# Kernel tuning notes

Hardware: AMD Instinct MI355X
Metric: run time of the kernel (lower is better)

## Reference

```python
import jax, jax.numpy as jnp
import numpy as np

B, S, H = 2, 2048, 2304
NH, NKV, HD = 8, 4, 256
SOFTCAP = 50.0
INIT = 0.02


def setup_inputs() -> dict:
    key = jax.random.key(0)
    k1, k2, k3, k4, k5 = jax.random.split(key, 5)
    hidden_states = jax.random.normal(k1, (B, S, H), dtype=jnp.float32)
    attention_mask = jnp.ones((B, S), dtype=jnp.int32)
    position_ids = jnp.broadcast_to(jnp.arange(S, dtype=jnp.int32), (B, S))
    Wq = jax.random.normal(k2, (H, NH * HD), dtype=jnp.float32) * INIT
    Wk = jax.random.normal(k3, (H, NKV * HD), dtype=jnp.float32) * INIT
    Wv = jax.random.normal(k4, (H, NKV * HD), dtype=jnp.float32) * INIT
    Wo = jax.random.normal(k5, (NH * HD, H), dtype=jnp.float32) * INIT
    return {"hidden_states": hidden_states, "attention_mask": attention_mask,
            "position_ids": position_ids, "Wq": Wq, "Wk": Wk, "Wv": Wv, "Wo": Wo}


def _rotate_half(t):
    return jnp.concatenate([-t[..., HD // 2:], t[..., :HD // 2]], axis=-1)


def reference(hidden_states, attention_mask, position_ids, Wq, Wk, Wv, Wo):
    b, s, _ = hidden_states.shape
    # projections + head split
    q = (hidden_states @ Wq).reshape(b, s, NH, HD)
    k = (hidden_states @ Wk).reshape(b, s, NKV, HD)
    v = (hidden_states @ Wv).reshape(b, s, NKV, HD)
    # RoPE (Gemma sinusoidal table, gathered by position_ids)
    inv_freq = 1.0 / (10000.0 ** (jnp.arange(0, HD, 2, dtype=jnp.float32) / HD))
    freqs = position_ids.astype(jnp.float32)[..., None] * inv_freq      # [B,S,HD/2]
    emb = jnp.concatenate([freqs, freqs], axis=-1)                      # [B,S,HD]
    sin = jnp.sin(emb)[:, :, None, :]
    cos = jnp.cos(emb)[:, :, None, :]
    q = q * cos + _rotate_half(q) * sin
    k = k * cos + _rotate_half(k) * sin
    # GQA: repeat KV heads to match query heads
    groups = NH // NKV
    k = jnp.repeat(k, groups, axis=2)
    v = jnp.repeat(v, groups, axis=2)
    # scaled logits, mask, tanh softcap (order matches source: mask -> softcap -> softmax)
    q = q / jnp.sqrt(jnp.float32(HD))
    scores = jnp.einsum('bqhd,bkhd->bhqk', q, k)                        # [B,NH,S,S]
    causal = jnp.tril(jnp.ones((s, s), dtype=bool))
    mask = causal[None, None] & (attention_mask[:, None, None, :] > 0)
    big_neg = jnp.finfo(scores.dtype).min
    scores = jnp.where(mask, scores, big_neg)
    scores = jnp.tanh(scores / SOFTCAP) * SOFTCAP
    w = jax.nn.softmax(scores, axis=-1)
    out = jnp.einsum('bhqk,bkhd->bqhd', w, v).reshape(b, s, NH * HD)
    return out @ Wo
```

## Files before the change

### kernel.cpp

```cpp
#include <hip/hip_runtime.h>
#include <hip/hip_bf16.h>
#include <stdint.h>

typedef unsigned short u16;
typedef __attribute__((ext_vector_type(8))) short s16x8;
typedef __attribute__((ext_vector_type(4))) float f32x4;

#define B_ 2
#define S_ 2048
#define H_ 2304
#define NH_ 8
#define NKV_ 4
#define HD_ 256

__device__ __forceinline__ float bf2f(u16 u) {
  union { uint32_t i; float f; } x; x.i = ((uint32_t)u) << 16; return x.f;
}
__device__ __forceinline__ u16 f2bf(float f) {
  union { float f; uint32_t i; } x; x.f = f;
  uint32_t u = x.i;
  return (u16)((u + 0x7fffu + ((u >> 16) & 1u)) >> 16);
}
__device__ __forceinline__ u16 f2bft(float f) {
  union { float f; uint32_t i; } x; x.f = f;
  return (u16)(x.i >> 16);
}

__device__ __forceinline__ void async16(const void* g, void* l) {
  __builtin_amdgcn_global_load_lds((const __attribute__((address_space(1))) uint32_t*)g,
                                   (__attribute__((address_space(3))) uint32_t*)l, 16, 0, 0);
}

__device__ __forceinline__ f32x4 mfma16(s16x8 a, s16x8 b, f32x4 c) {
  return __builtin_amdgcn_mfma_f32_16x16x32_bf16(a, b, c, 0, 0, 0);
}

__global__ __launch_bounds__(256) void prep_kernel(
    const float* __restrict__ X, u16* __restrict__ Xb,
    const float* __restrict__ Wq, u16* __restrict__ WqT,
    const float* __restrict__ Wk, u16* __restrict__ WkT,
    const float* __restrict__ Wv, u16* __restrict__ WvT,
    const float* __restrict__ Wo, u16* __restrict__ WoT,
    float* __restrict__ ct, float* __restrict__ st) {
  __shared__ u16 tile[32][33];
  int bid = blockIdx.x, tid = threadIdx.x;

  auto tposeT = [&](const float* in, u16* out, int R, int C, int bx, int by) {
    int c0 = bx * 32, r0 = by * 32;
    int x = tid & 31, y = tid >> 5;
#pragma unroll
    for (int j = 0; j < 32; j += 8)
      tile[y + j][x] = f2bf(in[(size_t)(r0 + y + j) * C + c0 + x]);
    __syncthreads();
#pragma unroll
    for (int j = 0; j < 32; j += 8)
      out[(size_t)(c0 + y + j) * R + r0 + x] = tile[x][y + j];
  };

  if (bid < 1024) {
    int t = bid * 256 + tid;
    int d = t & 127;
    int p = t >> 7;
    float invf = exp2f(-(float)d * 0.1038102530f);
    float f = (float)p * invf;
    float s, c;
    sincosf(f, &s, &c);
    ct[t] = c;
    st[t] = s;
  } else if (bid < 10240) {
    size_t i = ((size_t)(bid - 1024) * 256 + tid) * 4;
    float4 v = *(const float4*)(X + i);
    ushort4 o;
    o.x = f2bf(v.x); o.y = f2bf(v.y); o.z = f2bf(v.z); o.w = f2bf(v.w);
    *(ushort4*)(Xb + i) = o;
  } else if (bid < 14848) {
    int b2 = bid - 10240;
    tposeT(Wq, WqT, 2304, 2048, b2 & 63, b2 >> 6);
  } else if (bid < 17152) {
    int b2 = bid - 14848;
    tposeT(Wk, WkT, 2304, 1024, b2 & 31, b2 >> 5);
  } else if (bid < 19456) {
    int b2 = bid - 17152;
    tposeT(Wv, WvT, 2304, 1024, b2 & 31, b2 >> 5);
  } else {
    int b2 = bid - 19456;
    tposeT(Wo, WoT, 2048, 2304, b2 % 72, b2 / 72);
  }
}

__global__ __launch_bounds__(256) void mid_kernel(u16* __restrict__ QKV, u16* __restrict__ VTb,
                                                  const int* __restrict__ pos_ids,
                                                  const float* __restrict__ ct,
                                                  const float* __restrict__ st) {
  __shared__ u16 tile[32][33];
  int bid = blockIdx.x, tid = threadIdx.x;
  if (bid < 1024) {
    int t = bid * 256 + tid;
    int dg = t & 15, h = (t >> 4) & 3, row = t >> 6;
    u16* p1 = QKV + (size_t)row * 4096 + 2048 + h * 256 + dg * 8;
    u16* p2 = p1 + 128;
    int pos = pos_ids[row];
    const float* ctp = ct + pos * 128 + dg * 8;
    const float* stp = st + pos * 128 + dg * 8;
    s16x8 v1 = *(const s16x8*)p1, v2 = *(const s16x8*)p2;
#pragma unroll
    for (int j = 0; j < 8; j++) {
      float c = ctp[j], s = stp[j];
      float a = bf2f((u16)v1[j]);
      float b = bf2f((u16)v2[j]);
      v1[j] = (short)f2bf(a * c - b * s);
      v2[j] = (short)f2bf(b * c + a * s);
    }
    *(s16x8*)p1 = v1;
    *(s16x8*)p2 = v2;
  } else {
    int b2 = bid - 1024;
    int bx = b2 & 31;
    int by = (b2 >> 5) & 63;
    int z = b2 >> 11;
    const u16* in = QKV + 3072 + (size_t)z * 2048 * 4096;
    u16* out = VTb + (size_t)z * 1024 * 2048;
    int c0 = bx * 32, r0 = by * 32;
    int x = tid & 31, y = tid >> 5;
#pragma unroll
    for (int j = 0; j < 32; j += 8)
      tile[y + j][x] = in[(size_t)(r0 + y + j) * 4096 + c0 + x];
    __syncthreads();
#pragma unroll
    for (int j = 0; j < 32; j += 8)
      out[(size_t)(c0 + y + j) * 2048 + r0 + x] = tile[x][y + j];
  }
}

template <bool F32OUT>
__global__ __launch_bounds__(512) void gemm256(const u16* __restrict__ A, const u16* __restrict__ BT,
                                               void* __restrict__ Cout, int M, int N, int Kd) {
  __shared__ u16 As[2][256 * 64];
  __shared__ u16 Bs[2][256 * 64];
  int tid = threadIdx.x, lane = tid & 63, wave = tid >> 6;
  int nT = gridDim.x * gridDim.y;
  int bid = blockIdx.y * gridDim.x + blockIdx.x;
  int tile = (bid & 7) * (nT >> 3) + (bid >> 3);
  int bn = (tile % gridDim.x) * 256;
  int bm = (tile / gridDim.x) * 256;
  int wm = (wave >> 2) * 128, wn = (wave & 3) * 64;
  int fr = lane & 15, fq = lane >> 4;
  f32x4 acc[8][4];
#pragma unroll
  for (int i = 0; i < 8; i++)
#pragma unroll
    for (int j = 0; j < 4; j++) acc[i][j] = (f32x4){0.f, 0.f, 0.f, 0.f};

  int srow = tid >> 3, sslot = tid & 7;
  int scol = (sslot * 8) ^ ((srow & 7) << 3);
  const u16* Ab = A + (size_t)(bm + srow) * Kd + scol;
  const u16* Bb = BT + (size_t)(bn + srow) * Kd + scol;

  auto stage1 = [&](int buf, int k0, int i) {
    if (i < 4)
      async16(Ab + (size_t)i * 64 * Kd + k0, (char*)&As[buf][0] + wave * 1024 + i * 8192);
    else
      async16(Bb + (size_t)(i - 4) * 64 * Kd + k0, (char*)&Bs[buf][0] + wave * 1024 + (i - 4) * 8192);
  };

  int NT = Kd >> 6;
  int rsw = (fr & 7) << 3;
#pragma unroll
  for (int i = 0; i < 8; i++) stage1(0, 0, i);

  for (int t = 0; t < NT; ++t) {
    asm volatile("s_waitcnt vmcnt(0)" ::: "memory");
    __builtin_amdgcn_sched_barrier(0);
    __builtin_amdgcn_s_barrier();
    __builtin_amdgcn_sched_barrier(0);
    const u16* Ap = &As[t & 1][0];
    const u16* Bp = &Bs[t & 1][0];
    bool more = (t + 1 < NT);
    int nb = (t + 1) & 1;
    int nk = (t + 1) << 6;
    s16x8 bfr[4][2];
#pragma unroll
    for (int q = 0; q < 4; q++) {
      if (q == 0) {
#pragma unroll
        for (int j = 0; j < 4; j++)
#pragma unroll
          for (int s = 0; s < 2; s++)
            bfr[j][s] = *(const s16x8*)&Bp[(wn + j * 16 + fr) * 64 + ((s * 32 + fq * 8) ^ rsw)];
      }
      s16x8 aq[2][2];
#pragma unroll
      for (int rf = 0; rf < 2; rf++)
#pragma unroll
        for (int s = 0; s < 2; s++)
          aq[rf][s] = *(const s16x8*)&Ap[(wm + q * 32 + rf * 16 + fr) * 64 + ((s * 32 + fq * 8) ^ rsw)];
      if (more && q < 2) {
#pragma unroll
        for (int i = 0; i < 4; i++) stage1(nb, nk, q * 4 + i);
      }
      asm volatile("s_waitcnt lgkmcnt(0)" ::: "memory");
      __builtin_amdgcn_sched_barrier(0);
      __builtin_amdgcn_s_setprio(1);
#pragma unroll
      for (int rf = 0; rf < 2; rf++)
#pragma unroll
        for (int j = 0; j < 4; j++) {
          acc[q * 2 + rf][j] = mfma16(aq[rf][0], bfr[j][0], acc[q * 2 + rf][j]);
          acc[q * 2 + rf][j] = mfma16(aq[rf][1], bfr[j][1], acc[q * 2 + rf][j]);
        }
      __builtin_amdgcn_s_setprio(0);
      __builtin_amdgcn_sched_barrier(0);
    }
  }

#pragma unroll
  for (int i = 0; i < 8; i++)
#pragma unroll
    for (int j = 0; j < 4; j++)
#pragma unroll
      for (int r = 0; r < 4; r++) {
        int row = bm + wm + i * 16 + fq * 4 + r;
        int col = bn + wn + j * 16 + fr;
        if (F32OUT) ((float*)Cout)[(size_t)row * N + col] = acc[i][j][r];
        else        ((u16*)Cout)[(size_t)row * N + col] = f2bf(acc[i][j][r]);
      }
}

template <bool F32OUT>
__global__ __launch_bounds__(256) void gemm128(const u16* __restrict__ A, const u16* __restrict__ BT,
                                               void* __restrict__ Cout, int M, int N, int Kd) {
  __shared__ u16 As[2][128 * 32];
  __shared__ u16 Bs[2][128 * 32];
  int tid = threadIdx.x, lane = tid & 63, wave = tid >> 6;
  int nT = gridDim.x * gridDim.y;
  int bid = blockIdx.y * gridDim.x + blockIdx.x;
  int tile = (bid & 7) * (nT >> 3) + (bid >> 3);
  int bn = (tile % gridDim.x) * 128;
  int bm = (tile / gridDim.x) * 128;
  int wm = (wave >> 1) * 64, wn = (wave & 1) * 64;
  int fr = lane & 15, fq = lane >> 4;
  f32x4 acc[4][4];
#pragma unroll
  for (int i = 0; i < 4; i++)
#pragma unroll
    for (int j = 0; j < 4; j++) acc[i][j] = (f32x4){0.f, 0.f, 0.f, 0.f};

  int srow = tid >> 2, sslot = tid & 3;
  int scol = (sslot * 8) ^ ((srow & 3) << 3);
  const u16* Ab = A + (size_t)(bm + srow) * Kd + scol;
  const u16* Bb = BT + (size_t)(bn + srow) * Kd + scol;

  auto stage = [&](int buf, int k0) {
    async16(Ab + k0, (char*)&As[buf][0] + wave * 1024);
    async16(Ab + (size_t)64 * Kd + k0, (char*)&As[buf][0] + wave * 1024 + 4096);
    async16(Bb + k0, (char*)&Bs[buf][0] + wave * 1024);
    async16(Bb + (size_t)64 * Kd + k0, (char*)&Bs[buf][0] + wave * 1024 + 4096);
  };

  int NT = Kd >> 5;
  int rsw = (fr & 3) << 3;
  stage(0, 0);
  for (int t = 0; t < NT; ++t) {
    if (t + 1 < NT) {
      stage((t + 1) & 1, (t + 1) << 5);
      asm volatile("s_waitcnt vmcnt(4)" ::: "memory");
    } else {
      asm volatile("s_waitcnt vmcnt(0)" ::: "memory");
    }
    __builtin_amdgcn_sched_barrier(0);
    __builtin_amdgcn_s_barrier();
    __builtin_amdgcn_sched_barrier(0);
    const u16* Ap = &As[t & 1][0];
    const u16* Bp = &Bs[t & 1][0];
    __builtin_amdgcn_s_setprio(1);
    s16x8 af[4], bv[4];
#pragma unroll
    for (int i = 0; i < 4; i++) af[i] = *(const s16x8*)&Ap[(wm + i * 16 + fr) * 32 + ((fq * 8) ^ rsw)];
#pragma unroll
    for (int j = 0; j < 4; j++) bv[j] = *(const s16x8*)&Bp[(wn + j * 16 + fr) * 32 + ((fq * 8) ^ rsw)];
#pragma unroll
    for (int i = 0; i < 4; i++)
#pragma unroll
      for (int j = 0; j < 4; j++)
        acc[i][j] = mfma16(af[i], bv[j], acc[i][j]);
    __builtin_amdgcn_s_setprio(0);
    asm volatile("s_waitcnt lgkmcnt(0)" ::: "memory");
    __builtin_amdgcn_sched_barrier(0);
    __builtin_amdgcn_s_barrier();
  }
#pragma unroll
  for (int i = 0; i < 4; i++)
#pragma unroll
    for (int j = 0; j < 4; j++)
#pragma unroll
      for (int r = 0; r < 4; r++) {
        int row = bm + wm + i * 16 + fq * 4 + r;
        int col = bn + wn + j * 16 + fr;
        if (F32OUT) ((float*)Cout)[(size_t)row * N + col] = acc[i][j][r];
        else        ((u16*)Cout)[(size_t)row * N + col] = f2bf(acc[i][j][r]);
      }
}

__global__ __launch_bounds__(256) void attn_kernel(const u16* __restrict__ QKV, const u16* __restrict__ VT,
                                                   const int* __restrict__ amask, const int* __restrict__ pos_ids,
                                                   const float* __restrict__ ct, const float* __restrict__ st,
                                                   u16* __restrict__ O0, u16* __restrict__ O1,
                                                   float* __restrict__ L0, float* __restrict__ L1) {
  __shared__ u16 Kl[2][32 * 256];
  __shared__ u16 Vl[256 * 32];
  __shared__ u16 Pl[4][16 * 32];
  __shared__ unsigned char Mb[256];
  int id = blockIdx.x;
  int bg = id & 7;
  int r_ = id >> 3;
  int qt = 31 - (r_ >> 2);
  int hl = (r_ >> 1) & 1;
  int half = r_ & 1;
  int b = bg >> 2, g = bg & 3;
  int h = g * 2 + hl;
  int tid = threadIdx.x, lane = tid & 63, wave = tid >> 6;
  int fr = lane & 15, fq = lane >> 4;
  int q0 = qt * 64;
  u16* Op = half ? O1 : O0;
  float* Lp = half ? L1 : L0;

  const int* amp = amask + b * S_;
  {
    int4 a = *(const int4*)(amp + tid * 8);
    int4 c = *(const int4*)(amp + tid * 8 + 4);
    unsigned v = (unsigned)(a.x > 0) | ((unsigned)(a.y > 0) << 1) | ((unsigned)(a.z > 0) << 2) |
                 ((unsigned)(a.w > 0) << 3) | ((unsigned)(c.x > 0) << 4) | ((unsigned)(c.y > 0) << 5) |
                 ((unsigned)(c.z > 0) << 6) | ((unsigned)(c.w > 0) << 7);
    Mb[tid] = (unsigned char)v;
  }

  int qrow_g = b * S_ + q0 + wave * 16 + fr;
  s16x8 qr[8];
  const u16* qb = QKV + (size_t)qrow_g * 4096 + h * 256 + fq * 8;
#pragma unroll
  for (int kk = 0; kk < 8; kk++) qr[kk] = *(const s16x8*)(qb + kk * 32);
  int pos = pos_ids[qrow_g];
  const float* ctp = ct + pos * 128 + fq * 8;
  const float* stp = st + pos * 128 + fq * 8;
  s16x8 qf[8];
#pragma unroll
  for (int kk = 0; kk < 4; kk++) {
#pragma unroll
    for (int jj = 0; jj < 8; jj++) {
      float c = ctp[kk * 32 + jj], s = stp[kk * 32 + jj];
      float a = bf2f((u16)qr[kk][jj]);
      float bb = bf2f((u16)qr[kk + 4][jj]);
      qf[kk][jj]     = (short)f2bf((a * c - bb * s) * 0.0625f);
      qf[kk + 4][jj] = (short)f2bf((bb * c + a * s) * 0.0625f);
    }
  }

  f32x4 zero4 = {0.f, 0.f, 0.f, 0.f};
  f32x4 oacc[16];
#pragma unroll
  for (int i = 0; i < 16; i++) oacc[i] = zero4;
  f32x4 lacc = zero4;
  s16x8 onesv;
#pragma unroll
  for (int i = 0; i < 8; i++) onesv[i] = (short)0x3F80;

  const u16* Kbase = QKV + (size_t)b * S_ * 4096 + 2048 + g * 256;
  const u16* Vbase = VT + (size_t)(b * 4 + g) * 256 * S_;

  const u16* KsP[4];
  const u16* VsP[4];
  int dst16[4];
#pragma unroll
  for (int i = 0; i < 4; i++) {
    int c = tid + i * 256;
    int key = c >> 5, slot = c & 31;
    KsP[i] = Kbase + (size_t)key * 4096 + ((slot ^ (key & 7)) * 8);
    int hd = c >> 2, vs = c & 3;
    VsP[i] = Vbase + (size_t)hd * 2048 + ((vs ^ ((hd >> 1) & 3)) * 8);
    dst16[i] = c * 16;
  }

  __syncthreads();

#pragma unroll
  for (int i = 0; i < 4; i++)
    async16(KsP[i] + (size_t)(half * 32) * 4096, (char*)&Kl[0][0] + dst16[i]);

  int nt = 2 * qt + 2;
  int ksw = fr & 7;
  int vswl = (fr >> 1) & 3;
  int psw = (fr & 3) << 3;
  int kb = 0;
  for (int t = half; t < nt; t += 2) {
    int k0 = t * 32;
    bool more = (t + 2 < nt);
    asm volatile("s_waitcnt vmcnt(0)" ::: "memory");
    __builtin_amdgcn_sched_barrier(0);
    __builtin_amdgcn_s_barrier();
    __builtin_amdgcn_sched_barrier(0);

#pragma unroll
    for (int i = 0; i < 4; i++)
      async16(VsP[i] + k0, (char*)&Vl[0] + dst16[i]);
    if (more) {
#pragma unroll
      for (int i = 0; i < 4; i++)
        async16(KsP[i] + (size_t)(k0 + 64) * 4096, (char*)&Kl[kb ^ 1][0] + dst16[i]);
    }

    const u16* Kp = &Kl[kb][0];
    __builtin_amdgcn_s_setprio(1);
    f32x4 s0 = zero4, s1 = zero4;
#pragma unroll
    for (int kk = 0; kk < 8; kk++) {
      s16x8 b0 = *(const s16x8*)&Kp[fr * 256 + (((kk * 4 + fq) ^ ksw) * 8)];
      s16x8 b1 = *(const s16x8*)&Kp[(16 + fr) * 256 + (((kk * 4 + fq) ^ ksw) * 8)];
      s0 = mfma16(qf[kk], b0, s0);
      s1 = mfma16(qf[kk], b1, s1);
    }
    __builtin_amdgcn_s_setprio(0);

    int am0 = (Mb[(k0 + fr) >> 3] >> ((k0 + fr) & 7)) & 1;
    int am1 = (Mb[(k0 + 16 + fr) >> 3] >> ((k0 + 16 + fr) & 7)) & 1;
    bool needmask = (t >= nt - 2);
    float pv0[4], pv1[4];
#pragma unroll
    for (int r = 0; r < 4; r++) {
      float e20 = __expf(s0[r] * 0.04f);
      float e21 = __expf(s1[r] * 0.04f);
      pv0[r] = __expf(__fdividef(-100.f, e20 + 1.f));
      pv1[r] = __expf(__fdividef(-100.f, e21 + 1.f));
    }
    if (needmask) {
#pragma unroll
      for (int r = 0; r < 4; r++) {
        int qg = q0 + wave * 16 + fq * 4 + r;
        if (!((k0 + fr) <= qg)) pv0[r] = 0.f;
        if (!((k0 + 16 + fr) <= qg)) pv1[r] = 0.f;
      }
    }
#pragma unroll
    for (int r = 0; r < 4; r++) {
      int qrow = fq * 4 + r;
      float p0 = am0 ? pv0[r] : 0.f;
      float p1 = am1 ? pv1[r] : 0.f;
      Pl[wave][qrow * 32 + (fr ^ (r << 3))] = f2bft(p0);
      Pl[wave][qrow * 32 + ((16 + fr) ^ (r << 3))] = f2bft(p1);
    }
    asm volatile("s_waitcnt lgkmcnt(0)" ::: "memory");
    __builtin_amdgcn_sched_barrier(0);
    if (more)
      asm volatile("s_waitcnt vmcnt(4)" ::: "memory");
    else
      asm volatile("s_waitcnt vmcnt(0)" ::: "memory");
    __builtin_amdgcn_sched_barrier(0);
    __builtin_amdgcn_s_barrier();
    __builtin_amdgcn_sched_barrier(0);

    s16x8 pf = *(const s16x8*)&Pl[wave][fr * 32 + ((fq * 8) ^ psw)];
    __builtin_amdgcn_s_setprio(1);
    lacc = mfma16(pf, onesv, lacc);
#pragma unroll
    for (int df = 0; df < 16; df++) {
      s16x8 vv = *(const s16x8*)&Vl[(df * 16 + fr) * 32 + ((fq ^ vswl) * 8)];
      oacc[df] = mfma16(pf, vv, oacc[df]);
    }
    __builtin_amdgcn_s_setprio(0);
    asm volatile("s_waitcnt lgkmcnt(0)" ::: "memory");
    __builtin_amdgcn_sched_barrier(0);
    kb ^= 1;
  }

  if (fr == 0) {
#pragma unroll
    for (int r = 0; r < 4; r++)
      Lp[(size_t)(b * S_ + q0 + wave * 16 + fq * 4 + r) * 8 + h] = lacc[r];
  }
#pragma unroll
  for (int df = 0; df < 16; df++) {
#pragma unroll
    for (int r = 0; r < 4; r++) {
      Op[(size_t)(b * S_ + q0 + wave * 16 + fq * 4 + r) * 2048 + h * 256 + df * 16 + fr] =
          f2bf(oacc[df][r]);
    }
  }
}

__global__ void combine_o(const u16* __restrict__ O0, const u16* __restrict__ O1,
                          const float* __restrict__ L0, const float* __restrict__ L1,
                          u16* __restrict__ AO) {
  int idx = blockIdx.x * blockDim.x + threadIdx.x;
  int row = idx >> 8;
  int cg = idx & 255;
  int h = cg >> 5;
  float rinv = 1.0f / (L0[row * 8 + h] + L1[row * 8 + h]);
  size_t base = (size_t)row * 2048 + cg * 8;
  s16x8 a = *(const s16x8*)(O0 + base);
  s16x8 b = *(const s16x8*)(O1 + base);
  s16x8 o;
#pragma unroll
  for (int j = 0; j < 8; j++)
    o[j] = (short)f2bf((bf2f((u16)a[j]) + bf2f((u16)b[j])) * rinv);
  *(s16x8*)(AO + base) = o;
}

extern "C" void kernel_launch(void* const* d_in, const int* in_sizes, int n_in,
                              void* d_out, int out_size, void* d_ws, size_t ws_size,
                              hipStream_t stream) {
  const float* X   = (const float*)d_in[0];
  const int* amask = (const int*)d_in[1];
  const int* pos   = (const int*)d_in[2];
  const float* Wq  = (const float*)d_in[3];
  const float* Wk  = (const float*)d_in[4];
  const float* Wv  = (const float*)d_in[5];
  const float* Wo  = (const float*)d_in[6];
  float* out = (float*)d_out;

  char* ws = (char*)d_ws;
  size_t off = 0;
  auto allocB = [&](size_t bytes) {
    char* p = ws + off;
    off += ((bytes + 255) & ~(size_t)255);
    return p;
  };
  u16* Xb   = (u16*)allocB((size_t)4096 * 2304 * 2);
  u16* WqT  = (u16*)allocB((size_t)2048 * 2304 * 2);
  u16* WkT  = (u16*)allocB((size_t)1024 * 2304 * 2);
  u16* WvT  = (u16*)allocB((size_t)1024 * 2304 * 2);
  u16* WoT  = (u16*)allocB((size_t)2304 * 2048 * 2);
  u16* QKV  = (u16*)allocB((size_t)4096 * 4096 * 2);
  u16* VTb  = (u16*)allocB((size_t)4096 * 1024 * 2);
  u16* AO   = (u16*)allocB((size_t)4096 * 2048 * 2);
  float* CT = (float*)allocB((size_t)2048 * 128 * 4);
  float* ST = (float*)allocB((size_t)2048 * 128 * 4);
  float* Lp0 = (float*)allocB((size_t)4096 * 8 * 4);
  float* Lp1 = (float*)allocB((size_t)4096 * 8 * 4);
  u16* Op0 = (u16*)ws;
  u16* Op1 = Op0 + (size_t)4096 * 2048;
  if (off > ws_size) return;

  prep_kernel<<<24064, 256, 0, stream>>>(X, Xb, Wq, WqT, Wk, WkT, Wv, WvT, Wo, WoT, CT, ST);

  gemm256<false><<<dim3(4096 / 256, 4096 / 256), 512, 0, stream>>>(Xb, WqT, QKV, 4096, 4096, 2304);

  mid_kernel<<<5120, 256, 0, stream>>>(QKV, VTb, pos, CT, ST);

  attn_kernel<<<dim3(1024), 256, 0, stream>>>(QKV, VTb, amask, pos, CT, ST, Op0, Op1, Lp0, Lp1);

  combine_o<<<4096, 256, 0, stream>>>(Op0, Op1, Lp0, Lp1, AO);

  gemm128<true><<<dim3(2304 / 128, 4096 / 128), 256, 0, stream>>>(AO, WoT, out, 4096, 2304, 2048);
}
```

Before: 239.3 us.

## Interleave GEMM prefetch with MFMA phases and drop trailing barrier

The GEMM main loop is split into two half-phases. Each phase loads a pair of A fragments and issues two of the four async global-to-LDS copies for the next K tile, interleaved with the MFMA work. The end-of-iteration barrier is removed, leaving one barrier per iteration, with a full vmcnt(0) wait at the top. This aims to cut barrier overhead and spread memory issue across compute, but prefetches start later in the iteration, so there may be less latency hiding than the earlier stage-then-wait scheme.

```diff
diff --git a/kernel.cpp b/kernel.cpp
--- a/kernel.cpp
+++ b/kernel.cpp
@@ -250,43 +250,55 @@
   const u16* Ab = A + (size_t)(bm + srow) * Kd + scol;
   const u16* Bb = BT + (size_t)(bn + srow) * Kd + scol;
 
-  auto stage = [&](int buf, int k0) {
-    async16(Ab + k0, (char*)&As[buf][0] + wave * 1024);
-    async16(Ab + (size_t)64 * Kd + k0, (char*)&As[buf][0] + wave * 1024 + 4096);
-    async16(Bb + k0, (char*)&Bs[buf][0] + wave * 1024);
-    async16(Bb + (size_t)64 * Kd + k0, (char*)&Bs[buf][0] + wave * 1024 + 4096);
+  auto stage1 = [&](int buf, int k0, int i) {
+    if (i == 0)      async16(Ab + k0, (char*)&As[buf][0] + wave * 1024);
+    else if (i == 1) async16(Ab + (size_t)64 * Kd + k0, (char*)&As[buf][0] + wave * 1024 + 4096);
+    else if (i == 2) async16(Bb + k0, (char*)&Bs[buf][0] + wave * 1024);
+    else             async16(Bb + (size_t)64 * Kd + k0, (char*)&Bs[buf][0] + wave * 1024 + 4096);
   };
 
   int NT = Kd >> 5;
   int rsw = (fr & 3) << 3;
-  stage(0, 0);
+#pragma unroll
+  for (int i = 0; i < 4; i++) stage1(0, 0, i);
+
   for (int t = 0; t < NT; ++t) {
-    if (t + 1 < NT) {
-      stage((t + 1) & 1, (t + 1) << 5);
-      asm volatile("s_waitcnt vmcnt(4)" ::: "memory");
-    } else {
-      asm volatile("s_waitcnt vmcnt(0)" ::: "memory");
-    }
+    asm volatile("s_waitcnt vmcnt(0)" ::: "memory");
     __builtin_amdgcn_sched_barrier(0);
     __builtin_amdgcn_s_barrier();
     __builtin_amdgcn_sched_barrier(0);
     const u16* Ap = &As[t & 1][0];
     const u16* Bp = &Bs[t & 1][0];
-    __builtin_amdgcn_s_setprio(1);
-    s16x8 af[4], bv[4];
-#pragma unroll
-    for (int i = 0; i < 4; i++) af[i] = *(const s16x8*)&Ap[(wm + i * 16 + fr) * 32 + ((fq * 8) ^ rsw)];
-#pragma unroll
-    for (int j = 0; j < 4; j++) bv[j] = *(const s16x8*)&Bp[(wn + j * 16 + fr) * 32 + ((fq * 8) ^ rsw)];
-#pragma unroll
-    for (int i = 0; i < 4; i++)
-#pragma unroll
-      for (int j = 0; j < 4; j++)
-        acc[i][j] = mfma16(af[i], bv[j], acc[i][j]);
-    __builtin_amdgcn_s_setprio(0);
-    asm volatile("s_waitcnt lgkmcnt(0)" ::: "memory");
-    __builtin_amdgcn_sched_barrier(0);
-    __builtin_amdgcn_s_barrier();
+    bool more = (t + 1 < NT);
+    int nb = (t + 1) & 1;
+    int nk = (t + 1) << 5;
+    s16x8 bv[4];
+#pragma unroll
+    for (int q = 0; q < 2; q++) {
+      if (q == 0) {
+#pragma unroll
+        for (int j = 0; j < 4; j++)
+          bv[j] = *(const s16x8*)&Bp[(wn + j * 16 + fr) * 32 + ((fq * 8) ^ rsw)];
+      }
+      s16x8 aq[2];
+#pragma unroll
+      for (int rf = 0; rf < 2; rf++)
+        aq[rf] = *(const s16x8*)&Ap[(wm + (q * 2 + rf) * 16 + fr) * 32 + ((fq * 8) ^ rsw)];
+      if (more) {
+        stage1(nb, nk, q * 2);
+        stage1(nb, nk, q * 2 + 1);
+      }
+      asm volatile("s_waitcnt lgkmcnt(0)" ::: "memory");
+      __builtin_amdgcn_sched_barrier(0);
+      __builtin_amdgcn_s_setprio(1);
+#pragma unroll
+      for (int rf = 0; rf < 2; rf++)
+#pragma unroll
+        for (int j = 0; j < 4; j++)
+          acc[q * 2 + rf][j] = mfma16(aq[rf], bv[j], acc[q * 2 + rf][j]);
+      __builtin_amdgcn_s_setprio(0);
+      __builtin_amdgcn_sched_barrier(0);
+    }
   }
 #pragma unroll
   for (int i = 0; i < 4; i++)
```

Result: no change. 235.6 us (-1.5%).
